# Performance work log

Hardware: AMD Instinct MI355X
Metric: run time of the kernel (lower is better)

The kernel has to match this reference:

```python
import jax, jax.numpy as jnp
import numpy as np

B, TX, TY = 32, 64, 64
E = H = 1024
VEN = VCN = 32000


def _lstm_scan(x_gates, Whh, bhh, h0, c0):
    # x_gates: [T, B, 4H] precomputed input contribution (x @ Wih.T + bih)
    def step(carry, xg_t):
        h, c = carry
        gates = xg_t + h @ Whh.T + bhh  # [B, 4H]
        i, f, g, o = jnp.split(gates, 4, axis=-1)  # torch gate order i,f,g,o
        c = jax.nn.sigmoid(f) * c + jax.nn.sigmoid(i) * jnp.tanh(g)
        h = jax.nn.sigmoid(o) * jnp.tanh(c)
        return (h, c), (h, c)
    (hT, cT), (hs, cs) = jax.lax.scan(step, (h0, c0), x_gates)
    return hs, cs, hT, cT  # hs/cs: [T, B, H]


def setup_inputs() -> dict:
    key = jax.random.key(0)
    ks = jax.random.split(key, 12)
    u = lambda k, shp, s: jax.random.uniform(k, shp, jnp.float32, -s, s)
    s = 1.0 / np.sqrt(H)
    return {
        "x": jax.random.randint(ks[0], (B, TX), 0, VEN, dtype=jnp.int32),
        "x_mask": jnp.ones((B, TX), dtype=jnp.int32),
        "y": jax.random.randint(ks[1], (B, TY), 0, VCN, dtype=jnp.int32),
        "h0": jnp.zeros((B, H), jnp.float32),
        "c0": jnp.zeros((B, H), jnp.float32),
        "emb_en": u(ks[2], (VEN, E), 0.1),
        "emb_cn": u(ks[3], (VCN, E), 0.1),
        "Wih_e": u(ks[4], (4 * H, E), s),
        "Whh_e": u(ks[5], (4 * H, H), s),
        "bih_e": jnp.zeros((4 * H,), jnp.float32),
        "bhh_e": jnp.zeros((4 * H,), jnp.float32),
        "Wih_d": u(ks[6], (4 * H, E), s),
        "Whh_d": u(ks[7], (4 * H, H), s),
        "bih_d": jnp.zeros((4 * H,), jnp.float32),
        "bhh_d": jnp.zeros((4 * H,), jnp.float32),
        "Wout": u(ks[8], (VCN, H), 0.1),
        "bout": jnp.zeros((VCN,), jnp.float32),
    }


def reference(x, x_mask, y, h0, c0, emb_en, emb_cn,
              Wih_e, Whh_e, bih_e, bhh_e,
              Wih_d, Whh_d, bih_d, bhh_d, Wout, bout):
    # --- encoder: per-timestep LSTMCell unrolled via lax.scan ---
    xe = emb_en[x]  # [B, Tx, E]
    xg = jnp.einsum('bte,ge->tbg', xe, Wih_e) + bih_e  # [Tx, B, 4H]
    hs, cs, _, _ = _lstm_scan(xg, Whh_e, bhh_e, h0, c0)  # [Tx, B, H]
    # pick hidden/cell at last valid timestep (mask.sum - 1)
    lengths = jnp.sum(x_mask, axis=1) - 1  # [B]
    bidx = jnp.arange(x.shape[0])
    h = hs[lengths, bidx]  # [B, H]
    c = cs[lengths, bidx]
    # --- decoder: single-layer LSTM ---
    ye = emb_cn[y]  # [B, Ty, E]
    yg = jnp.einsum('bte,ge->tbg', ye, Wih_d) + bih_d  # [Ty, B, 4H]
    dh, _, _, _ = _lstm_scan(yg, Whh_d, bhh_d, h, c)  # [Ty, B, H]
    hiddens = jnp.transpose(dh, (1, 0, 2))  # [B, Ty, H]
    logits = jnp.einsum('bth,vh->btv', hiddens, Wout) + bout  # [B, Ty, V]
    decoded = jax.nn.log_softmax(logits, axis=-1)
    return decoded, hiddens
```

## Files before the change

### kernel.cpp

```cpp
#include <hip/hip_runtime.h>

typedef __attribute__((ext_vector_type(8))) short bf16x8;
typedef __attribute__((ext_vector_type(4))) float fx4;
typedef __attribute__((ext_vector_type(4))) unsigned short u16x4;
typedef __attribute__((ext_vector_type(8))) unsigned short u16x8;
typedef __attribute__((ext_vector_type(4))) unsigned int u32x4;

#define DEV static __device__ __forceinline__

DEV unsigned short f2bf(float f) {
  union { float f; unsigned u; } v; v.f = f;
  unsigned u = v.u;
  u += 0x7fffu + ((u >> 16) & 1u);
  return (unsigned short)(u >> 16);
}
DEV unsigned pk(float a, float b) { return (unsigned)f2bf(a) | ((unsigned)f2bf(b) << 16); }
DEV float sigm(float x) { return 1.f / (1.f + __expf(-x)); }

DEV u32x4 load_coh16(const void* p) {
  u32x4 r;
  asm volatile("global_load_dwordx4 %0, %1, off sc0 sc1" : "=v"(r) : "v"(p));
  return r;
}

typedef __attribute__((address_space(1))) const unsigned int guint;
typedef __attribute__((address_space(3))) unsigned int luint;
DEV void gload_lds16(const void* g, void* l) {
  __builtin_amdgcn_global_load_lds((guint*)g, (luint*)l, 16, 0, 0);
}

__global__ void k_f2bf4(const float* __restrict__ s, unsigned short* __restrict__ d, long n4) {
  long i = (long)blockIdx.x * blockDim.x + threadIdx.x;
  long st = (long)gridDim.x * blockDim.x;
  for (; i < n4; i += st) {
    fx4 v = ((const fx4*)s)[i];
    u16x4 o = { f2bf(v[0]), f2bf(v[1]), f2bf(v[2]), f2bf(v[3]) };
    ((u16x4*)d)[i] = o;
  }
}

__global__ void k_gather(const float* __restrict__ emb, const int* __restrict__ tok,
                         unsigned short* __restrict__ dst) {
  int r = blockIdx.x;
  int t = r >> 5, b = r & 31;
  int token = tok[b * 64 + t];
  const fx4* srow = (const fx4*)(emb + (long)token * 1024);
  u16x4* drow = (u16x4*)(dst + (long)r * 1024);
  fx4 v = srow[threadIdx.x];
  u16x4 o = { f2bf(v[0]), f2bf(v[1]), f2bf(v[2]), f2bf(v[3]) };
  drow[threadIdx.x] = o;
}

__global__ void k_lengths(const int* __restrict__ mask, int* __restrict__ sel) {
  int b = threadIdx.x;
  if (b < 32) {
    int s = 0;
    for (int t = 0; t < 64; ++t) s += mask[b * 64 + t];
    sel[b] = (s + 63) & 63;
  }
}

__global__ void k_init_state(const float* __restrict__ h, const float* __restrict__ c,
                             unsigned short* __restrict__ hbuf0, float* __restrict__ cbuf,
                             int* __restrict__ bar) {
  int i = blockIdx.x * 256 + threadIdx.x;
  hbuf0[i] = f2bf(h[i]);
  cbuf[i] = c[i];
  if (i < 4096) bar[i] = 0;
}

#define SCAN_NBLK 128

template<int MODE>
__global__ __launch_bounds__(512) void k_scan(
    const float* __restrict__ Whh,
    const float* __restrict__ bhh,
    const float* __restrict__ xg,
    unsigned short* __restrict__ hbuf,
    float* __restrict__ cbuf,
    const int* __restrict__ sel,
    float* __restrict__ hsel, float* __restrict__ csel,
    float* __restrict__ hid_out,
    unsigned short* __restrict__ hid_bf,
    int* __restrict__ bar) {
  __shared__ __align__(16) unsigned short hlds[49152];
  __shared__ float gbuf[2][2][32][16];
  int tid = threadIdx.x;
  int bid = blockIdx.x;
  int j0 = bid * 8;
  int w = tid >> 6, lane = tid & 63;
  int mt = w & 1, nt = (w >> 1) & 1, kh = w >> 2;
  int fr = lane & 15, fg = lane >> 4;
  unsigned* hbU = (unsigned*)hbuf;

  bf16x8 breg[16];
  {
    int r = nt * 16 + fr;
    const float* wrow = Whh + ((long)((r >> 3) * 1024 + j0 + (r & 7)) << 10);
#pragma unroll
    for (int i = 0; i < 16; ++i) {
      int kc = (kh * 16 + i) * 4 + fg;
      fx4 lo = *(const fx4*)(wrow + kc * 8);
      fx4 hi = *(const fx4*)(wrow + kc * 8 + 4);
      bf16x8 o = { (short)f2bf(lo[0]), (short)f2bf(lo[1]), (short)f2bf(lo[2]), (short)f2bf(lo[3]),
                   (short)f2bf(hi[0]), (short)f2bf(hi[1]), (short)f2bf(hi[2]), (short)f2bf(hi[3]) };
      breg[i] = o;
    }
  }

  int b = (tid & 255) >> 3, jj = tid & 7, j = j0 + jj;
  float bh0 = 0.f, bh1 = 0.f, bh2 = 0.f, bh3 = 0.f, c_reg = 0.f;
  float x0 = 0.f, x1 = 0.f, x2 = 0.f, x3 = 0.f;
  int sel_b = -1;
  if (tid < 256) {
    bh0 = bhh[j]; bh1 = bhh[1024 + j]; bh2 = bhh[2048 + j]; bh3 = bhh[3072 + j];
    c_reg = cbuf[b * 1024 + j];
    if (MODE == 0) sel_b = sel[b];
    const float* xp = xg + (long)b * 4096 + j;
    x0 = xp[0]; x1 = xp[1024]; x2 = xp[2048]; x3 = xp[3072];
  }

  for (int t = 0; t < 64; ++t) {
    const char* hsrc = (const char*)hbuf + (t & 1) * 65536;
    u32x4 hv[8];
#pragma unroll
    for (int it = 0; it < 8; ++it) {
      int c = it * 512 + tid;
      hv[it] = load_coh16(hsrc + (long)c * 16);
    }
    asm volatile("s_waitcnt vmcnt(0)" ::: "memory");
    __builtin_amdgcn_sched_barrier(0);
#pragma unroll
    for (int it = 0; it < 8; ++it) {
      int c = it * 512 + tid;
      int row = c >> 7, kc = c & 127;
      *(u16x8*)&hlds[(row * 128 + (kc ^ (row & 31))) * 8] = *(u16x8*)&hv[it];
    }
    __syncthreads();

    int arow = mt * 16 + fr;
    fx4 acca = {0.f, 0.f, 0.f, 0.f}, accb = {0.f, 0.f, 0.f, 0.f};
#pragma unroll
    for (int i = 0; i < 16; i += 2) {
      int kcA = (kh * 16 + i) * 4 + fg;
      int kcB = (kh * 16 + i + 1) * 4 + fg;
      bf16x8 a0 = *(const bf16x8*)&hlds[(arow * 128 + (kcA ^ (arow & 31))) * 8];
      bf16x8 a1 = *(const bf16x8*)&hlds[(arow * 128 + (kcB ^ (arow & 31))) * 8];
      acca = __builtin_amdgcn_mfma_f32_16x16x32_bf16(a0, breg[i], acca, 0, 0, 0);
      accb = __builtin_amdgcn_mfma_f32_16x16x32_bf16(a1, breg[i + 1], accb, 0, 0, 0);
    }
#pragma unroll
    for (int q = 0; q < 4; ++q)
      gbuf[kh][nt][mt * 16 + fg * 4 + q][fr] = acca[q] + accb[q];
    __syncthreads();

    if (tid < 256) {
      float gi = gbuf[0][0][b][jj]     + gbuf[1][0][b][jj]     + bh0 + x0;
      float gf = gbuf[0][0][b][8 + jj] + gbuf[1][0][b][8 + jj] + bh1 + x1;
      float gg = gbuf[0][1][b][jj]     + gbuf[1][1][b][jj]     + bh2 + x2;
      float go = gbuf[0][1][b][8 + jj] + gbuf[1][1][b][8 + jj] + bh3 + x3;
      float c_new = sigm(gf) * c_reg + sigm(gi) * tanhf(gg);
      float h = sigm(go) * tanhf(c_new);
      c_reg = c_new;
      float hp = __shfl_xor(h, 1);
      if ((jj & 1) == 0) {
        unsigned val = pk(h, hp);
        __hip_atomic_store(&hbU[((t & 1) ^ 1) * 16384 + b * 512 + ((j0 + jj) >> 1)], val,
                           __ATOMIC_RELAXED, __HIP_MEMORY_SCOPE_AGENT);
      }
      if (MODE == 0) {
        if (t == sel_b) { hsel[b * 1024 + j] = h; csel[b * 1024 + j] = c_new; }
      } else {
        long o = ((long)b * 64 + t) * 1024 + j;
        hid_out[o] = h;
        if (hid_bf) hid_bf[o] = f2bf(h);
      }
    }

    if (t < 63) {
      float nx0 = 0.f, nx1 = 0.f, nx2 = 0.f, nx3 = 0.f;
      if (tid < 256) {
        const float* xp = xg + (long)(t + 1) * 131072 + (long)b * 4096 + j;
        nx0 = xp[0]; nx1 = xp[1024]; nx2 = xp[2048]; nx3 = xp[3072];
      }
      __syncthreads();
      if (w == 0) {
        if (lane == 0)
          __hip_atomic_store(&bar[bid * 32], t + 1, __ATOMIC_RELAXED, __HIP_MEMORY_SCOPE_AGENT);
        for (;;) {
          int v0 = __hip_atomic_load(&bar[lane * 32], __ATOMIC_RELAXED, __HIP_MEMORY_SCOPE_AGENT);
          int v1 = __hip_atomic_load(&bar[(64 + lane) * 32], __ATOMIC_RELAXED, __HIP_MEMORY_SCOPE_AGENT);
          if (__ballot(v0 >= t + 1 && v1 >= t + 1) == 0xFFFFFFFFFFFFFFFFULL) break;
          __builtin_amdgcn_s_sleep(2);
        }
      }
      __syncthreads();
      x0 = nx0; x1 = nx1; x2 = nx2; x3 = nx3;
    }
  }
}

__global__ __launch_bounds__(256) void k_gemm_bb(const unsigned short* __restrict__ A,
                                                 const unsigned short* __restrict__ Bw,
                                                 const float* __restrict__ bias,
                                                 float* __restrict__ C,
                                                 int ldc, int q8) {
  __shared__ __align__(16) unsigned short As[2][4096];
  __shared__ __align__(16) unsigned short Bs[2][4096];
  int lid = blockIdx.x;
  int swz = (lid & 7) * q8 + (lid >> 3);
  long m0 = (long)(swz & 15) * 128;
  long n0 = (long)(swz >> 4) * 128;
  int tid = threadIdx.x, lane = tid & 63, w = tid >> 6;
  int mw = (w & 1) * 64, nw = (w >> 1) * 64;
  int fr = lane & 15, fg = lane >> 4;
  fx4 acc[4][4] = {};
  int c0 = tid, c1 = tid + 256;
  const unsigned short* gA0 = A + (m0 + (c0 >> 2)) * 1024 + (c0 & 3) * 8;
  const unsigned short* gA1 = A + (m0 + (c1 >> 2)) * 1024 + (c1 & 3) * 8;
  const unsigned short* gB0 = Bw + (n0 + (c0 >> 2)) * 1024 + (c0 & 3) * 8;
  const unsigned short* gB1 = Bw + (n0 + (c1 >> 2)) * 1024 + (c1 & 3) * 8;
  auto stage = [&](int buf, int kt) {
    int k0 = kt * 32;
    gload_lds16(gA0 + k0, &As[buf][c0 * 8]);
    gload_lds16(gA1 + k0, &As[buf][c1 * 8]);
    gload_lds16(gB0 + k0, &Bs[buf][c0 * 8]);
    gload_lds16(gB1 + k0, &Bs[buf][c1 * 8]);
  };
  stage(0, 0);
  __syncthreads();
  for (int kt = 0; kt < 32; ++kt) {
    int cur = kt & 1;
    if (kt < 31) stage(cur ^ 1, kt + 1);
    bf16x8 af[4], bfr[4];
#pragma unroll
    for (int mi = 0; mi < 4; ++mi) af[mi]  = *(const bf16x8*)&As[cur][(mw + mi * 16 + fr) * 32 + fg * 8];
#pragma unroll
    for (int ni = 0; ni < 4; ++ni) bfr[ni] = *(const bf16x8*)&Bs[cur][(nw + ni * 16 + fr) * 32 + fg * 8];
#pragma unroll
    for (int mi = 0; mi < 4; ++mi)
#pragma unroll
      for (int ni = 0; ni < 4; ++ni)
        acc[mi][ni] = __builtin_amdgcn_mfma_f32_16x16x32_bf16(af[mi], bfr[ni], acc[mi][ni], 0, 0, 0);
    __syncthreads();
  }
#pragma unroll
  for (int ni = 0; ni < 4; ++ni) {
    long n = n0 + nw + ni * 16 + fr;
    float bs = bias[n];
#pragma unroll
    for (int mi = 0; mi < 4; ++mi) {
      long rbase = m0 + mw + mi * 16 + fg * 4;
#pragma unroll
      for (int q = 0; q < 4; ++q)
        C[(rbase + q) * ldc + n] = acc[mi][ni][q] + bs;
    }
  }
}

template<typename TA, typename TB>
__global__ __launch_bounds__(256) void k_gemm(const TA* __restrict__ A,
                                              const TB* __restrict__ Bw,
                                              const float* __restrict__ bias,
                                              float* __restrict__ C,
                                              int ldc, int q8) {
  __shared__ __align__(16) unsigned short As[2][4096];
  __shared__ __align__(16) unsigned short Bs[2][4096];
  int lid = blockIdx.x;
  int swz = (lid & 7) * q8 + (lid >> 3);
  long m0 = (long)(swz & 15) * 128;
  long n0 = (long)(swz >> 4) * 128;
  int tid = threadIdx.x, lane = tid & 63, w = tid >> 6;
  int mw = (w & 1) * 64, nw = (w >> 1) * 64;
  int fr = lane & 15, fg = lane >> 4;
  fx4 acc[4][4] = {};

  int crow[2], kc[2], phys[2];
#pragma unroll
  for (int u = 0; u < 2; ++u) {
    int c = tid + u * 256;
    crow[u] = c >> 2; kc[u] = c & 3;
    phys[u] = crow[u] * 4 + (kc[u] ^ ((crow[u] >> 1) & 3));
  }
  u32x4 ra[2], rb[2];
  auto loadOne = [&](const auto* P, long row, int u) -> u32x4 {
    long off = row * 1024 + kc[u] * 8;
    if constexpr (sizeof(*P) == 2) {
      return *(const u32x4*)(P + off);
    } else {
      fx4 lo = *(const fx4*)(P + off);
      fx4 hi = *(const fx4*)(P + off + 4);
      u32x4 r = { pk(lo[0], lo[1]), pk(lo[2], lo[3]), pk(hi[0], hi[1]), pk(hi[2], hi[3]) };
      return r;
    }
  };
  auto loadRegs = [&](int kt) {
#pragma unroll
    for (int u = 0; u < 2; ++u) {
      ra[u] = loadOne(A + (long)kt * 32, m0 + crow[u], u);
      rb[u] = loadOne(Bw + (long)kt * 32, n0 + crow[u], u);
    }
  };
  auto storeRegs = [&](int buf) {
#pragma unroll
    for (int u = 0; u < 2; ++u) {
      *(u32x4*)&As[buf][phys[u] * 8] = ra[u];
      *(u32x4*)&Bs[buf][phys[u] * 8] = rb[u];
    }
  };
  loadRegs(0);
  storeRegs(0);
  __syncthreads();
  for (int kt = 0; kt < 32; ++kt) {
    int cur = kt & 1;
    if (kt < 31) loadRegs(kt + 1);
    bf16x8 af[4], bf_[4];
#pragma unroll
    for (int mi = 0; mi < 4; ++mi) {
      int row = mw + mi * 16 + fr;
      af[mi] = *(const bf16x8*)&As[cur][(row * 4 + (fg ^ ((row >> 1) & 3))) * 8];
    }
#pragma unroll
    for (int ni = 0; ni < 4; ++ni) {
      int row = nw + ni * 16 + fr;
      bf_[ni] = *(const bf16x8*)&Bs[cur][(row * 4 + (fg ^ ((row >> 1) & 3))) * 8];
    }
#pragma unroll
    for (int mi = 0; mi < 4; ++mi)
#pragma unroll
      for (int ni = 0; ni < 4; ++ni)
        acc[mi][ni] = __builtin_amdgcn_mfma_f32_16x16x32_bf16(af[mi], bf_[ni], acc[mi][ni], 0, 0, 0);
    if (kt < 31) storeRegs((kt + 1) & 1);
    __syncthreads();
  }
#pragma unroll
  for (int ni = 0; ni < 4; ++ni) {
    long n = n0 + nw + ni * 16 + fr;
    float bs = bias[n];
#pragma unroll
    for (int mi = 0; mi < 4; ++mi) {
      long rbase = m0 + mw + mi * 16 + fg * 4;
#pragma unroll
      for (int q = 0; q < 4; ++q)
        C[(rbase + q) * ldc + n] = acc[mi][ni][q] + bs;
    }
  }
}

__global__ __launch_bounds__(256) void k_logsoftmax(float* __restrict__ logits) {
  long base = (long)blockIdx.x * 32000;
  float* row = logits + base;
  int tid = threadIdx.x;
  __shared__ float redm[4], reds[4];
  float m = -3.4e38f, s = 0.f;
  for (int i = tid; i < 8000; i += 256) {
    fx4 v = ((const fx4*)row)[i];
    float cm = fmaxf(fmaxf(v[0], v[1]), fmaxf(v[2], v[3]));
    if (cm > m) { s *= __expf(m - cm); m = cm; }
    s += __expf(v[0] - m) + __expf(v[1] - m) + __expf(v[2] - m) + __expf(v[3] - m);
  }
  for (int o = 32; o; o >>= 1) {
    float m2 = __shfl_xor(m, o), s2 = __shfl_xor(s, o);
    float mn = fmaxf(m, m2);
    s = s * __expf(m - mn) + s2 * __expf(m2 - mn);
    m = mn;
  }
  if ((tid & 63) == 0) { redm[tid >> 6] = m; reds[tid >> 6] = s; }
  __syncthreads();
  float M = fmaxf(fmaxf(redm[0], redm[1]), fmaxf(redm[2], redm[3]));
  float S = reds[0] * __expf(redm[0] - M) + reds[1] * __expf(redm[1] - M) +
            reds[2] * __expf(redm[2] - M) + reds[3] * __expf(redm[3] - M);
  float lse = M + logf(S);
  for (int i = tid; i < 8000; i += 256) {
    fx4 v = ((const fx4*)row)[i];
    fx4 o = { v[0] - lse, v[1] - lse, v[2] - lse, v[3] - lse };
    ((fx4*)row)[i] = o;
  }
}

extern "C" void kernel_launch(void* const* d_in, const int* in_sizes, int n_in,
                              void* d_out, int out_size, void* d_ws, size_t ws_size,
                              hipStream_t stream) {
  const int*   x     = (const int*)d_in[0];
  const int*   xmask = (const int*)d_in[1];
  const int*   y     = (const int*)d_in[2];
  const float* h0    = (const float*)d_in[3];
  const float* c0    = (const float*)d_in[4];
  const float* embE  = (const float*)d_in[5];
  const float* embC  = (const float*)d_in[6];
  const float* WihE  = (const float*)d_in[7];
  const float* WhhE  = (const float*)d_in[8];
  const float* bihE  = (const float*)d_in[9];
  const float* bhhE  = (const float*)d_in[10];
  const float* WihD  = (const float*)d_in[11];
  const float* WhhD  = (const float*)d_in[12];
  const float* bihD  = (const float*)d_in[13];
  const float* bhhD  = (const float*)d_in[14];
  const float* Wout  = (const float*)d_in[15];
  const float* bout  = (const float*)d_in[16];

  float* out = (float*)d_out;
  float* decoded = out;
  float* hiddens = out + 65536000L;

  float* xg_e = decoded;
  float* xg_d = decoded + 8388608L;
  unsigned short* xe_bf   = (unsigned short*)(decoded + 16777216L);
  unsigned short* ye_bf   = xe_bf + 2097152L;
  unsigned short* WihE_bf = ye_bf + 2097152L;
  unsigned short* WihD_bf = WihE_bf + 4194304L;
  char* sp = (char*)(WihD_bf + 4194304L);
  unsigned short* hbuf = (unsigned short*)sp; sp += 2 * 32768 * 2;
  float* cbuf = (float*)sp; sp += 32768 * 4;
  float* hsel = (float*)sp; sp += 32768 * 4;
  float* csel = (float*)sp; sp += 32768 * 4;
  int* sel = (int*)sp; sp += 256;
  int* bar = (int*)sp; sp += 16384;

  unsigned short* hid_bf  = (unsigned short*)d_ws;
  unsigned short* Wout_bf = hid_bf + 2097152L;
  bool fast1 = ws_size >= 2048L * 1024 * 2;
  bool fast2 = ws_size >= 2048L * 1024 * 2 + 32000L * 1024 * 2;

  k_gather<<<2048, 256, 0, stream>>>(embE, x, xe_bf);
  k_gather<<<2048, 256, 0, stream>>>(embC, y, ye_bf);
  k_lengths<<<1, 32, 0, stream>>>(xmask, sel);
  k_f2bf4<<<1024, 256, 0, stream>>>(WihE, WihE_bf, 4096L * 1024 / 4);
  k_f2bf4<<<1024, 256, 0, stream>>>(WihD, WihD_bf, 4096L * 1024 / 4);
  if (fast2) k_f2bf4<<<4096, 256, 0, stream>>>(Wout, Wout_bf, 32000L * 1024 / 4);

  k_gemm_bb<<<512, 256, 0, stream>>>(xe_bf, WihE_bf, bihE, xg_e, 4096, 64);
  k_gemm_bb<<<512, 256, 0, stream>>>(ye_bf, WihD_bf, bihD, xg_d, 4096, 64);

  k_init_state<<<128, 256, 0, stream>>>(h0, c0, hbuf, cbuf, bar);
  k_scan<0><<<SCAN_NBLK, 512, 0, stream>>>(WhhE, bhhE, xg_e, hbuf, cbuf, sel,
                                           hsel, csel, nullptr, nullptr, bar);
  k_init_state<<<128, 256, 0, stream>>>(hsel, csel, hbuf, cbuf, bar);
  k_scan<1><<<SCAN_NBLK, 512, 0, stream>>>(WhhD, bhhD, xg_d, hbuf, cbuf, nullptr,
                                           nullptr, nullptr, hiddens,
                                           fast1 ? hid_bf : nullptr, bar);

  if (fast2)      k_gemm_bb<<<4000, 256, 0, stream>>>(hid_bf, Wout_bf, bout, decoded, 32000, 500);
  else if (fast1) k_gemm<unsigned short, float><<<4000, 256, 0, stream>>>(hid_bf, Wout, bout, decoded, 32000, 500);
  else            k_gemm<float, float><<<4000, 256, 0, stream>>>(hiddens, Wout, bout, decoded, 32000, 500);
  k_logsoftmax<<<2048, 256, 0, stream>>>(decoded);
}
```

Measured before the change: 934.9 us.

## Fuse setup launches, overlap Wout conversion with scan, split log-softmax into GEMM epilogue

Merges the gather, weight-conversion and input GEMM launches into dual kernels, and folds state initialisation into the scan kernels so no init kernels run between them. Extra blocks in the encoder scan convert Wout to bf16 while the recurrence runs, and the scan block-to-column mapping is permuted. The output GEMM now writes per-tile row max and sum-exp partials, which a small LSE kernel combines so the final pass is only a subtraction instead of a full log-softmax over the logits. The risks are contention between the conversion blocks and the persistent scan's spin barrier, and a dependence on workspace size for the fast path.

```diff
diff --git a/kernel.cpp b/kernel.cpp
--- a/kernel.cpp
+++ b/kernel.cpp
@@ -29,19 +29,15 @@
   __builtin_amdgcn_global_load_lds((guint*)g, (luint*)l, 16, 0, 0);
 }
 
-__global__ void k_f2bf4(const float* __restrict__ s, unsigned short* __restrict__ d, long n4) {
-  long i = (long)blockIdx.x * blockDim.x + threadIdx.x;
-  long st = (long)gridDim.x * blockDim.x;
-  for (; i < n4; i += st) {
-    fx4 v = ((const fx4*)s)[i];
-    u16x4 o = { f2bf(v[0]), f2bf(v[1]), f2bf(v[2]), f2bf(v[3]) };
-    ((u16x4*)d)[i] = o;
-  }
-}
-
-__global__ void k_gather(const float* __restrict__ emb, const int* __restrict__ tok,
-                         unsigned short* __restrict__ dst) {
-  int r = blockIdx.x;
+__global__ void k_gather2(const float* __restrict__ embE, const int* __restrict__ tokE,
+                          unsigned short* __restrict__ dstE,
+                          const float* __restrict__ embC, const int* __restrict__ tokC,
+                          unsigned short* __restrict__ dstC) {
+  int bid = blockIdx.x;
+  int r = bid & 2047;
+  const float* emb = bid < 2048 ? embE : embC;
+  const int* tok = bid < 2048 ? tokE : tokC;
+  unsigned short* dst = bid < 2048 ? dstE : dstC;
   int t = r >> 5, b = r & 31;
   int token = tok[b * 64 + t];
   const fx4* srow = (const fx4*)(emb + (long)token * 1024);
@@ -51,22 +47,28 @@
   drow[threadIdx.x] = o;
 }
 
-__global__ void k_lengths(const int* __restrict__ mask, int* __restrict__ sel) {
-  int b = threadIdx.x;
-  if (b < 32) {
+__global__ void k_lengths(const int* __restrict__ mask, int* __restrict__ sel,
+                          int* __restrict__ bar) {
+  int t = threadIdx.x;
+  for (int i = t; i < 4096; i += 256) bar[i] = 0;
+  if (t < 32) {
     int s = 0;
-    for (int t = 0; t < 64; ++t) s += mask[b * 64 + t];
-    sel[b] = (s + 63) & 63;
-  }
-}
-
-__global__ void k_init_state(const float* __restrict__ h, const float* __restrict__ c,
-                             unsigned short* __restrict__ hbuf0, float* __restrict__ cbuf,
-                             int* __restrict__ bar) {
-  int i = blockIdx.x * 256 + threadIdx.x;
-  hbuf0[i] = f2bf(h[i]);
-  cbuf[i] = c[i];
-  if (i < 4096) bar[i] = 0;
+    for (int k = 0; k < 64; ++k) s += mask[t * 64 + k];
+    sel[t] = (s + 63) & 63;
+  }
+}
+
+__global__ void k_f2bf_dual(const float* __restrict__ s0, unsigned short* __restrict__ d0,
+                            const float* __restrict__ s1, unsigned short* __restrict__ d1,
+                            long n4) {
+  const float* s = blockIdx.x < 1024 ? s0 : s1;
+  unsigned short* d = blockIdx.x < 1024 ? d0 : d1;
+  long base = (long)(blockIdx.x & 1023) * 256 + threadIdx.x;
+  for (long i = base; i < n4; i += 1024 * 256) {
+    fx4 v = ((const fx4*)s)[i];
+    u16x4 o = { f2bf(v[0]), f2bf(v[1]), f2bf(v[2]), f2bf(v[3]) };
+    ((u16x4*)d)[i] = o;
+  }
 }
 
 #define SCAN_NBLK 128
@@ -76,22 +78,37 @@
     const float* __restrict__ Whh,
     const float* __restrict__ bhh,
     const float* __restrict__ xg,
+    const float* __restrict__ hinit,
+    const float* __restrict__ cinit,
     unsigned short* __restrict__ hbuf,
-    float* __restrict__ cbuf,
     const int* __restrict__ sel,
     float* __restrict__ hsel, float* __restrict__ csel,
     float* __restrict__ hid_out,
     unsigned short* __restrict__ hid_bf,
-    int* __restrict__ bar) {
+    int* __restrict__ bar,
+    const float* __restrict__ wsrc,
+    unsigned short* __restrict__ wdst,
+    long wn4) {
+  int tid = threadIdx.x;
+  int bid = blockIdx.x;
+  if (bid >= SCAN_NBLK) {
+    long i = (long)(bid - SCAN_NBLK) * 512 + tid;
+    long st = (long)(gridDim.x - SCAN_NBLK) * 512;
+    for (; i < wn4; i += st) {
+      fx4 v = ((const fx4*)wsrc)[i];
+      u16x4 o = { f2bf(v[0]), f2bf(v[1]), f2bf(v[2]), f2bf(v[3]) };
+      ((u16x4*)wdst)[i] = o;
+    }
+    return;
+  }
   __shared__ __align__(16) unsigned short hlds[49152];
   __shared__ float gbuf[2][2][32][16];
-  int tid = threadIdx.x;
-  int bid = blockIdx.x;
-  int j0 = bid * 8;
+  int j0 = ((bid & 7) * 16 + (bid >> 3)) * 8;
   int w = tid >> 6, lane = tid & 63;
   int mt = w & 1, nt = (w >> 1) & 1, kh = w >> 2;
   int fr = lane & 15, fg = lane >> 4;
   unsigned* hbU = (unsigned*)hbuf;
+  constexpr int GBASE = MODE ? 64 : 0;
 
   bf16x8 breg[16];
   {
@@ -114,27 +131,41 @@
   int sel_b = -1;
   if (tid < 256) {
     bh0 = bhh[j]; bh1 = bhh[1024 + j]; bh2 = bhh[2048 + j]; bh3 = bhh[3072 + j];
-    c_reg = cbuf[b * 1024 + j];
+    c_reg = cinit[b * 1024 + j];
     if (MODE == 0) sel_b = sel[b];
     const float* xp = xg + (long)b * 4096 + j;
     x0 = xp[0]; x1 = xp[1024]; x2 = xp[2048]; x3 = xp[3072];
   }
 
   for (int t = 0; t < 64; ++t) {
-    const char* hsrc = (const char*)hbuf + (t & 1) * 65536;
-    u32x4 hv[8];
-#pragma unroll
-    for (int it = 0; it < 8; ++it) {
-      int c = it * 512 + tid;
-      hv[it] = load_coh16(hsrc + (long)c * 16);
-    }
-    asm volatile("s_waitcnt vmcnt(0)" ::: "memory");
-    __builtin_amdgcn_sched_barrier(0);
-#pragma unroll
-    for (int it = 0; it < 8; ++it) {
-      int c = it * 512 + tid;
-      int row = c >> 7, kc = c & 127;
-      *(u16x8*)&hlds[(row * 128 + (kc ^ (row & 31))) * 8] = *(u16x8*)&hv[it];
+    if (t == 0) {
+#pragma unroll
+      for (int it = 0; it < 8; ++it) {
+        int c = it * 512 + tid;
+        const float* src = hinit + (long)c * 8;
+        fx4 lo = *(const fx4*)src;
+        fx4 hi = *(const fx4*)(src + 4);
+        int row = c >> 7, kc = c & 127;
+        u16x8 o = { f2bf(lo[0]), f2bf(lo[1]), f2bf(lo[2]), f2bf(lo[3]),
+                    f2bf(hi[0]), f2bf(hi[1]), f2bf(hi[2]), f2bf(hi[3]) };
+        *(u16x8*)&hlds[(row * 128 + (kc ^ (row & 31))) * 8] = o;
+      }
+    } else {
+      const char* hsrc = (const char*)hbuf + (t & 1) * 65536;
+      u32x4 hv[8];
+#pragma unroll
+      for (int it = 0; it < 8; ++it) {
+        int c = it * 512 + tid;
+        hv[it] = load_coh16(hsrc + (long)c * 16);
+      }
+      asm volatile("s_waitcnt vmcnt(0)" ::: "memory");
+      __builtin_amdgcn_sched_barrier(0);
+#pragma unroll
+      for (int it = 0; it < 8; ++it) {
+        int c = it * 512 + tid;
+        int row = c >> 7, kc = c & 127;
+        *(u16x8*)&hlds[(row * 128 + (kc ^ (row & 31))) * 8] = *(u16x8*)&hv[it];
+      }
     }
     __syncthreads();
 
@@ -186,12 +217,13 @@
       __syncthreads();
       if (w == 0) {
         if (lane == 0)
-          __hip_atomic_store(&bar[bid * 32], t + 1, __ATOMIC_RELAXED, __HIP_MEMORY_SCOPE_AGENT);
+          __hip_atomic_store(&bar[bid * 32], GBASE + t + 1, __ATOMIC_RELAXED, __HIP_MEMORY_SCOPE_AGENT);
+        int want = GBASE + t + 1;
         for (;;) {
           int v0 = __hip_atomic_load(&bar[lane * 32], __ATOMIC_RELAXED, __HIP_MEMORY_SCOPE_AGENT);
           int v1 = __hip_atomic_load(&bar[(64 + lane) * 32], __ATOMIC_RELAXED, __HIP_MEMORY_SCOPE_AGENT);
-          if (__ballot(v0 >= t + 1 && v1 >= t + 1) == 0xFFFFFFFFFFFFFFFFULL) break;
-          __builtin_amdgcn_s_sleep(2);
+          if (__ballot(v0 >= want && v1 >= want) == 0xFFFFFFFFFFFFFFFFULL) break;
+          __builtin_amdgcn_s_sleep(1);
         }
       }
       __syncthreads();
@@ -200,15 +232,20 @@
   }
 }
 
-__global__ __launch_bounds__(256) void k_gemm_bb(const unsigned short* __restrict__ A,
-                                                 const unsigned short* __restrict__ Bw,
-                                                 const float* __restrict__ bias,
-                                                 float* __restrict__ C,
-                                                 int ldc, int q8) {
+__global__ __launch_bounds__(256) void k_gemm_dual(
+    const unsigned short* __restrict__ A0, const unsigned short* __restrict__ B0,
+    const float* __restrict__ bias0, float* __restrict__ C0,
+    const unsigned short* __restrict__ A1, const unsigned short* __restrict__ B1,
+    const float* __restrict__ bias1, float* __restrict__ C1) {
   __shared__ __align__(16) unsigned short As[2][4096];
   __shared__ __align__(16) unsigned short Bs[2][4096];
   int lid = blockIdx.x;
-  int swz = (lid & 7) * q8 + (lid >> 3);
+  int half = lid >> 9, l = lid & 511;
+  const unsigned short* A = half ? A1 : A0;
+  const unsigned short* Bw = half ? B1 : B0;
+  const float* bias = half ? bias1 : bias0;
+  float* C = half ? C1 : C0;
+  int swz = (l & 7) * 64 + (l >> 3);
   long m0 = (long)(swz & 15) * 128;
   long n0 = (long)(swz >> 4) * 128;
   int tid = threadIdx.x, lane = tid & 63, w = tid >> 6;
@@ -253,8 +290,160 @@
       long rbase = m0 + mw + mi * 16 + fg * 4;
 #pragma unroll
       for (int q = 0; q < 4; ++q)
-        C[(rbase + q) * ldc + n] = acc[mi][ni][q] + bs;
-    }
+        C[(rbase + q) * 4096 + n] = acc[mi][ni][q] + bs;
+    }
+  }
+}
+
+__global__ __launch_bounds__(256) void k_gemm_sp(const unsigned short* __restrict__ A,
+                                                 const unsigned short* __restrict__ Bw,
+                                                 const float* __restrict__ bias,
+                                                 float* __restrict__ C,
+                                                 float* __restrict__ pm,
+                                                 float* __restrict__ ps) {
+  __shared__ __align__(16) unsigned short As[2][4096];
+  __shared__ __align__(16) unsigned short Bs[2][4096];
+  __shared__ float redm[2][128], reds[2][128];
+  int lid = blockIdx.x;
+  int swz = (lid & 7) * 500 + (lid >> 3);
+  long m0 = (long)(swz & 15) * 128;
+  long n0 = (long)(swz >> 4) * 128;
+  int nb = swz >> 4;
+  int tid = threadIdx.x, lane = tid & 63, w = tid >> 6;
+  int mw = (w & 1) * 64, nw = (w >> 1) * 64;
+  int fr = lane & 15, fg = lane >> 4;
+  fx4 acc[4][4] = {};
+  int c0 = tid, c1 = tid + 256;
+  const unsigned short* gA0 = A + (m0 + (c0 >> 2)) * 1024 + (c0 & 3) * 8;
+  const unsigned short* gA1 = A + (m0 + (c1 >> 2)) * 1024 + (c1 & 3) * 8;
+  const unsigned short* gB0 = Bw + (n0 + (c0 >> 2)) * 1024 + (c0 & 3) * 8;
+  const unsigned short* gB1 = Bw + (n0 + (c1 >> 2)) * 1024 + (c1 & 3) * 8;
+  auto stage = [&](int buf, int kt) {
+    int k0 = kt * 32;
+    gload_lds16(gA0 + k0, &As[buf][c0 * 8]);
+    gload_lds16(gA1 + k0, &As[buf][c1 * 8]);
+    gload_lds16(gB0 + k0, &Bs[buf][c0 * 8]);
+    gload_lds16(gB1 + k0, &Bs[buf][c1 * 8]);
+  };
+  stage(0, 0);
+  __syncthreads();
+  for (int kt = 0; kt < 32; ++kt) {
+    int cur = kt & 1;
+    if (kt < 31) stage(cur ^ 1, kt + 1);
+    bf16x8 af[4], bfr[4];
+#pragma unroll
+    for (int mi = 0; mi < 4; ++mi) af[mi]  = *(const bf16x8*)&As[cur][(mw + mi * 16 + fr) * 32 + fg * 8];
+#pragma unroll
+    for (int ni = 0; ni < 4; ++ni) bfr[ni] = *(const bf16x8*)&Bs[cur][(nw + ni * 16 + fr) * 32 + fg * 8];
+#pragma unroll
+    for (int mi = 0; mi < 4; ++mi)
+#pragma unroll
+      for (int ni = 0; ni < 4; ++ni)
+        acc[mi][ni] = __builtin_amdgcn_mfma_f32_16x16x32_bf16(af[mi], bfr[ni], acc[mi][ni], 0, 0, 0);
+    __syncthreads();
+  }
+#pragma unroll
+  for (int ni = 0; ni < 4; ++ni) {
+    long n = n0 + nw + ni * 16 + fr;
+    float bs = bias[n];
+#pragma unroll
+    for (int mi = 0; mi < 4; ++mi) {
+      long rbase = m0 + mw + mi * 16 + fg * 4;
+#pragma unroll
+      for (int q = 0; q < 4; ++q) {
+        acc[mi][ni][q] += bs;
+        C[(rbase + q) * 32000 + n] = acc[mi][ni][q];
+      }
+    }
+  }
+  if (!pm) return;
+  float lmax[4][4];
+#pragma unroll
+  for (int mi = 0; mi < 4; ++mi)
+#pragma unroll
+    for (int q = 0; q < 4; ++q)
+      lmax[mi][q] = fmaxf(fmaxf(acc[mi][0][q], acc[mi][1][q]), fmaxf(acc[mi][2][q], acc[mi][3][q]));
+#pragma unroll
+  for (int off = 1; off < 16; off <<= 1)
+#pragma unroll
+    for (int mi = 0; mi < 4; ++mi)
+#pragma unroll
+      for (int q = 0; q < 4; ++q)
+        lmax[mi][q] = fmaxf(lmax[mi][q], __shfl_xor(lmax[mi][q], off));
+  if (fr == 0)
+#pragma unroll
+    for (int mi = 0; mi < 4; ++mi)
+#pragma unroll
+      for (int q = 0; q < 4; ++q)
+        redm[w >> 1][mw + mi * 16 + fg * 4 + q] = lmax[mi][q];
+  __syncthreads();
+  float rm[4][4], ls[4][4];
+#pragma unroll
+  for (int mi = 0; mi < 4; ++mi)
+#pragma unroll
+    for (int q = 0; q < 4; ++q) {
+      int R = mw + mi * 16 + fg * 4 + q;
+      rm[mi][q] = fmaxf(redm[0][R], redm[1][R]);
+      ls[mi][q] = __expf(acc[mi][0][q] - rm[mi][q]) + __expf(acc[mi][1][q] - rm[mi][q]) +
+                  __expf(acc[mi][2][q] - rm[mi][q]) + __expf(acc[mi][3][q] - rm[mi][q]);
+    }
+#pragma unroll
+  for (int off = 1; off < 16; off <<= 1)
+#pragma unroll
+    for (int mi = 0; mi < 4; ++mi)
+#pragma unroll
+      for (int q = 0; q < 4; ++q)
+        ls[mi][q] += __shfl_xor(ls[mi][q], off);
+  if (fr == 0)
+#pragma unroll
+    for (int mi = 0; mi < 4; ++mi)
+#pragma unroll
+      for (int q = 0; q < 4; ++q)
+        reds[w >> 1][mw + mi * 16 + fg * 4 + q] = ls[mi][q];
+  __syncthreads();
+  if ((w >> 1) == 0 && fr == 0) {
+#pragma unroll
+    for (int mi = 0; mi < 4; ++mi)
+#pragma unroll
+      for (int q = 0; q < 4; ++q) {
+        int R = mw + mi * 16 + fg * 4 + q;
+        long row = m0 + R;
+        pm[row * 250 + nb] = rm[mi][q];
+        ps[row * 250 + nb] = reds[0][R] + reds[1][R];
+      }
+  }
+}
+
+__global__ __launch_bounds__(256) void k_lse(const float* __restrict__ pm,
+                                             const float* __restrict__ ps,
+                                             float* __restrict__ lse) {
+  int w = threadIdx.x >> 6, lane = threadIdx.x & 63;
+  int row = blockIdx.x * 4 + w;
+  float m = -3.4e38f, s = 0.f;
+  for (int i = lane; i < 250; i += 64) {
+    float pmv = pm[(long)row * 250 + i], psv = ps[(long)row * 250 + i];
+    float mn = fmaxf(m, pmv);
+    s = s * __expf(m - mn) + psv * __expf(pmv - mn);
+    m = mn;
+  }
+  for (int off = 32; off; off >>= 1) {
+    float m2 = __shfl_xor(m, off), s2 = __shfl_xor(s, off);
+    float mn = fmaxf(m, m2);
+    s = s * __expf(m - mn) + s2 * __expf(m2 - mn);
+    m = mn;
+  }
+  if (lane == 0) lse[row] = m + logf(s);
+}
+
+__global__ __launch_bounds__(256) void k_norm(float* __restrict__ logits,
+                                              const float* __restrict__ lse) {
+  long base = (long)blockIdx.x * 32000;
+  float* row = logits + base;
+  float l = lse[blockIdx.x];
+  for (int i = threadIdx.x; i < 8000; i += 256) {
+    fx4 v = ((const fx4*)row)[i];
+    fx4 o = { v[0] - l, v[1] - l, v[2] - l, v[3] - l };
+    ((fx4*)row)[i] = o;
   }
 }
 
@@ -411,7 +600,6 @@
   unsigned short* WihD_bf = WihE_bf + 4194304L;
   char* sp = (char*)(WihD_bf + 4194304L);
   unsigned short* hbuf = (unsigned short*)sp; sp += 2 * 32768 * 2;
-  float* cbuf = (float*)sp; sp += 32768 * 4;
   float* hsel = (float*)sp; sp += 32768 * 4;
   float* csel = (float*)sp; sp += 32768 * 4;
   int* sel = (int*)sp; sp += 256;
@@ -419,29 +607,42 @@
 
   unsigned short* hid_bf  = (unsigned short*)d_ws;
   unsigned short* Wout_bf = hid_bf + 2097152L;
-  bool fast1 = ws_size >= 2048L * 1024 * 2;
-  bool fast2 = ws_size >= 2048L * 1024 * 2 + 32000L * 1024 * 2;
-
-  k_gather<<<2048, 256, 0, stream>>>(embE, x, xe_bf);
-  k_gather<<<2048, 256, 0, stream>>>(embC, y, ye_bf);
-  k_lengths<<<1, 32, 0, stream>>>(xmask, sel);
-  k_f2bf4<<<1024, 256, 0, stream>>>(WihE, WihE_bf, 4096L * 1024 / 4);
-  k_f2bf4<<<1024, 256, 0, stream>>>(WihD, WihD_bf, 4096L * 1024 / 4);
-  if (fast2) k_f2bf4<<<4096, 256, 0, stream>>>(Wout, Wout_bf, 32000L * 1024 / 4);
-
-  k_gemm_bb<<<512, 256, 0, stream>>>(xe_bf, WihE_bf, bihE, xg_e, 4096, 64);
-  k_gemm_bb<<<512, 256, 0, stream>>>(ye_bf, WihD_bf, bihD, xg_d, 4096, 64);
-
-  k_init_state<<<128, 256, 0, stream>>>(h0, c0, hbuf, cbuf, bar);
-  k_scan<0><<<SCAN_NBLK, 512, 0, stream>>>(WhhE, bhhE, xg_e, hbuf, cbuf, sel,
-                                           hsel, csel, nullptr, nullptr, bar);
-  k_init_state<<<128, 256, 0, stream>>>(hsel, csel, hbuf, cbuf, bar);
-  k_scan<1><<<SCAN_NBLK, 512, 0, stream>>>(WhhD, bhhD, xg_d, hbuf, cbuf, nullptr,
-                                           nullptr, nullptr, hiddens,
-                                           fast1 ? hid_bf : nullptr, bar);
-
-  if (fast2)      k_gemm_bb<<<4000, 256, 0, stream>>>(hid_bf, Wout_bf, bout, decoded, 32000, 500);
-  else if (fast1) k_gemm<unsigned short, float><<<4000, 256, 0, stream>>>(hid_bf, Wout, bout, decoded, 32000, 500);
-  else            k_gemm<float, float><<<4000, 256, 0, stream>>>(hiddens, Wout, bout, decoded, 32000, 500);
-  k_logsoftmax<<<2048, 256, 0, stream>>>(decoded);
-}
+  float* pm  = (float*)(Wout_bf + 32768000L);
+  float* psum = pm + 512000L;
+  float* lse = psum + 512000L;
+  size_t need1 = 2048L * 1024 * 2;
+  size_t need2 = need1 + 32000L * 1024 * 2;
+  size_t need3 = need2 + 512000L * 8 + 8192;
+  bool fast1 = ws_size >= need1;
+  bool fast2 = ws_size >= need2;
+  bool fast3 = ws_size >= need3;
+
+  k_gather2<<<4096, 256, 0, stream>>>(embE, x, xe_bf, embC, y, ye_bf);
+  k_lengths<<<1, 256, 0, stream>>>(xmask, sel, bar);
+  k_f2bf_dual<<<2048, 256, 0, stream>>>(WihE, WihE_bf, WihD, WihD_bf, 1048576L);
+
+  k_gemm_dual<<<1024, 256, 0, stream>>>(xe_bf, WihE_bf, bihE, xg_e,
+                                        ye_bf, WihD_bf, bihD, xg_d);
+
+  k_scan<0><<<SCAN_NBLK + (fast2 ? 112 : 0), 512, 0, stream>>>(
+      WhhE, bhhE, xg_e, h0, c0, hbuf, sel, hsel, csel, nullptr, nullptr, bar,
+      Wout, Wout_bf, fast2 ? 8192000L : 0L);
+  k_scan<1><<<SCAN_NBLK, 512, 0, stream>>>(
+      WhhD, bhhD, xg_d, hsel, csel, hbuf, nullptr, nullptr, nullptr, hiddens,
+      fast1 ? hid_bf : nullptr, bar, nullptr, nullptr, 0L);
+
+  if (fast3) {
+    k_gemm_sp<<<4000, 256, 0, stream>>>(hid_bf, Wout_bf, bout, decoded, pm, psum);
+    k_lse<<<512, 256, 0, stream>>>(pm, psum, lse);
+    k_norm<<<2048, 256, 0, stream>>>(decoded, lse);
+  } else if (fast2) {
+    k_gemm_sp<<<4000, 256, 0, stream>>>(hid_bf, Wout_bf, bout, decoded, nullptr, nullptr);
+    k_logsoftmax<<<2048, 256, 0, stream>>>(decoded);
+  } else if (fast1) {
+    k_gemm<unsigned short, float><<<4000, 256, 0, stream>>>(hid_bf, Wout, bout, decoded, 32000, 500);
+    k_logsoftmax<<<2048, 256, 0, stream>>>(decoded);
+  } else {
+    k_gemm<float, float><<<4000, 256, 0, stream>>>(hiddens, Wout, bout, decoded, 32000, 500);
+    k_logsoftmax<<<2048, 256, 0, stream>>>(decoded);
+  }
+}
```

New measurement: 977.5 us. +4.6%, slower.
